# Optimization experiments

Hardware: AMD Instinct MI355X
Metric: run time of the kernel (lower is better)

## Reference

```python
import jax, jax.numpy as jnp
import numpy as np

NUM_HEADS = 16
NUM_KV_HEADS = 4
HEAD_DIM = 128
ROPE_DIMS = 64
EPS = 1.1920929e-07  # torch.finfo(float32).eps, used by F.rms_norm(eps=None)


def rms_norm(x):
    ms = jnp.mean(jnp.square(x), axis=-1, keepdims=True)
    return x * jax.lax.rsqrt(ms + EPS)


def apply_rotary(x, cos, sin):
    # x: [..., s, rope_dims]; cos/sin: [s, rope_dims//2]
    h = x.shape[-1] // 2
    x1, x2 = x[..., :h], x[..., h:]
    return jnp.concatenate([x1 * cos + x2 * sin, -x1 * sin + x2 * cos], axis=-1)


def setup_inputs() -> dict:
    key = jax.random.key(0)
    ks = jax.random.split(key, 5)
    b, s, d = 2, 2048, 2048
    return {
        "x": jax.random.normal(ks[0], (b, s, d), jnp.float32),
        "q_w": jax.random.normal(ks[1], (d, d), jnp.float32) * 0.02,
        "k_w": jax.random.normal(ks[2], (NUM_KV_HEADS * HEAD_DIM, d), jnp.float32) * 0.02,
        "v_w": jax.random.normal(ks[3], (NUM_KV_HEADS * HEAD_DIM, d), jnp.float32) * 0.02,
        "out_w": jax.random.normal(ks[4], (d, d), jnp.float32) * 0.02,
        "q_gain": jnp.full((NUM_HEADS,), 12.0, jnp.float32),
    }


def reference(x, q_w, k_w, v_w, out_w, q_gain):
    b, s, d = x.shape
    g = NUM_HEADS // NUM_KV_HEADS

    q = (x @ q_w.T).reshape(b, s, NUM_HEADS, HEAD_DIM).transpose(0, 2, 1, 3)
    k = (x @ k_w.T).reshape(b, s, NUM_KV_HEADS, HEAD_DIM).transpose(0, 2, 1, 3)
    v = (x @ v_w.T).reshape(b, s, NUM_KV_HEADS, HEAD_DIM).transpose(0, 2, 1, 3)

    q = rms_norm(q)
    k = rms_norm(k)

    # partial rotary embedding
    t = jnp.arange(s, dtype=jnp.float32)
    inv_freq = 1.0 / (10000.0 ** (jnp.arange(0, ROPE_DIMS, 2, dtype=jnp.float32) / ROPE_DIMS))
    f = jnp.outer(t, inv_freq)                      # [s, rope_dims//2]
    cos, sin = jnp.cos(f), jnp.sin(f)

    q = jnp.concatenate([apply_rotary(q[..., :ROPE_DIMS], cos, sin), q[..., ROPE_DIMS:]], axis=-1)
    q = q * q_gain[None, :, None, None]
    k = jnp.concatenate([apply_rotary(k[..., :ROPE_DIMS], cos, sin), k[..., ROPE_DIMS:]], axis=-1)

    # GQA-native causal attention (no repeated K/V materialization)
    qg = q.reshape(b, NUM_KV_HEADS, g, s, HEAD_DIM)
    scale = 1.0 / jnp.sqrt(jnp.float32(HEAD_DIM))
    scores = jnp.einsum("bkgqd,bkld->bkgql", qg, k) * scale
    causal = jnp.tril(jnp.ones((s, s), bool))
    scores = jnp.where(causal, scores, jnp.finfo(scores.dtype).min)
    p = jax.nn.softmax(scores, axis=-1)
    y = jnp.einsum("bkgql,bkld->bkgqd", p, v)       # [b, kvh, g, s, hd]
    y = y.reshape(b, NUM_HEADS, s, HEAD_DIM).transpose(0, 2, 1, 3).reshape(b, s, d)
    return y @ out_w.T
```

## Files before the change

kernel.cpp:

```cpp
#include <hip/hip_runtime.h>
#include <cmath>


#define S_LEN 2048
#define DMODEL 2048
#define NH 16
#define NKV 4
#define HD 128

#define NEG_SENT -1.0e30f
#define QK_SCALE 0.08838834764831845f

typedef _Float16 f16x8 __attribute__((ext_vector_type(8)));
typedef float f32x4 __attribute__((ext_vector_type(4)));

static __device__ __forceinline__ short f2h(float f) {
  _Float16 h = (_Float16)f;
  return *(short*)&h;
}
static __device__ __forceinline__ float h2f(short s) {
  _Float16 h = *(_Float16*)&s;
  return (float)h;
}

__global__ __launch_bounds__(256) void f32_to_f16(const float* __restrict__ src,
                                                  short* __restrict__ dst, int n) {
  int i = (blockIdx.x * 256 + threadIdx.x) * 4;
  if (i < n) {
    float4 v = *reinterpret_cast<const float4*>(src + i);
    short4 o;
    o.x = f2h(v.x); o.y = f2h(v.y); o.z = f2h(v.z); o.w = f2h(v.w);
    *reinterpret_cast<short4*>(dst + i) = o;
  }
}

template <bool F32OUT>
__global__ __launch_bounds__(256) void gemm_bt(const short* __restrict__ A,
                                               const short* __restrict__ W,
                                               void* __restrict__ Cv,
                                               int M, int N, int K) {
  __shared__ __align__(16) short As[128][72];
  __shared__ __align__(16) short Ws[128][72];
  const int tid = threadIdx.x;
  const int wave = tid >> 6, lane = tid & 63;
  const int quad = lane >> 4, l16 = lane & 15;
  const int bm = blockIdx.x * 128, bn = blockIdx.y * 128;
  const int wm = (wave >> 1) * 64, wn = (wave & 1) * 64;

  f32x4 acc[4][4];
#pragma unroll
  for (int i = 0; i < 4; i++)
#pragma unroll
    for (int j = 0; j < 4; j++) acc[i][j] = f32x4{0.f, 0.f, 0.f, 0.f};

  const int lrow = tid >> 3;
  const int lcol = (tid & 7) * 8;

  for (int k0 = 0; k0 < K; k0 += 64) {
    __syncthreads();
#pragma unroll
    for (int i = 0; i < 4; i++) {
      int r = lrow + i * 32;
      *reinterpret_cast<int4*>(&As[r][lcol]) =
          *reinterpret_cast<const int4*>(A + (size_t)(bm + r) * K + k0 + lcol);
      *reinterpret_cast<int4*>(&Ws[r][lcol]) =
          *reinterpret_cast<const int4*>(W + (size_t)(bn + r) * K + k0 + lcol);
    }
    __syncthreads();
#pragma unroll
    for (int kk = 0; kk < 64; kk += 32) {
      f16x8 af[4], bfr[4];
#pragma unroll
      for (int mi = 0; mi < 4; mi++)
        af[mi] = *reinterpret_cast<const f16x8*>(&As[wm + mi * 16 + l16][kk + quad * 8]);
#pragma unroll
      for (int ni = 0; ni < 4; ni++)
        bfr[ni] = *reinterpret_cast<const f16x8*>(&Ws[wn + ni * 16 + l16][kk + quad * 8]);
#pragma unroll
      for (int mi = 0; mi < 4; mi++)
#pragma unroll
        for (int ni = 0; ni < 4; ni++)
          acc[mi][ni] = __builtin_amdgcn_mfma_f32_16x16x32_f16(af[mi], bfr[ni], acc[mi][ni], 0, 0, 0);
    }
  }
#pragma unroll
  for (int mi = 0; mi < 4; mi++)
#pragma unroll
    for (int ni = 0; ni < 4; ni++) {
      int gr = bm + wm + mi * 16 + quad * 4;
      int gc = bn + wn + ni * 16 + l16;
#pragma unroll
      for (int r = 0; r < 4; r++) {
        if (F32OUT)
          ((float*)Cv)[(size_t)(gr + r) * N + gc] = acc[mi][ni][r];
        else
          ((short*)Cv)[(size_t)(gr + r) * N + gc] = f2h(acc[mi][ni][r]);
      }
    }
}

__global__ __launch_bounds__(256) void postproc(const short* __restrict__ src,
                                                short* __restrict__ dst,
                                                const float* __restrict__ gain,
                                                int n_heads, int mode) {
  int gw = blockIdx.x * 4 + (threadIdx.x >> 6);
  int lane = threadIdx.x & 63;
  int head = gw % n_heads;
  int token = gw / n_heads;
  int s = token & (S_LEN - 1);
  int b = token >> 11;
  const short* sp = src + (size_t)token * (n_heads * HD) + head * HD;
  float v0 = h2f(sp[lane]);
  float v1 = h2f(sp[lane + 64]);
  float ss = v0 * v0 + v1 * v1;
#pragma unroll
  for (int off = 1; off < 64; off <<= 1) ss += __shfl_xor(ss, off, 64);
  float sc = rsqrtf(ss * (1.0f / 128.0f) + 1.1920929e-07f);
  v0 *= sc;
  v1 *= sc;
  int i = lane & 31;
  float inv = powf(10000.0f, -((float)(2 * i) * (1.0f / 64.0f)));
  float f = (float)s * inv;
  float cs, sn;
  sincosf(f, &sn, &cs);
  float partner = __shfl_xor(v0, 32, 64);
  v0 = (lane < 32) ? (v0 * cs + partner * sn) : (v0 * cs - partner * sn);
  if (mode == 2) {
    float g = gain[head] * QK_SCALE;
    v0 *= g;
    v1 *= g;
  }
  short* dp = dst + ((size_t)(b * n_heads + head) * S_LEN + s) * HD;
  dp[lane] = f2h(v0);
  dp[lane + 64] = f2h(v1);
}

__global__ __launch_bounds__(256) void v_transpose(const short* __restrict__ src,
                                                   short* __restrict__ dst) {
  __shared__ __align__(16) short t[64][72];
  const int tid = threadIdx.x;
  const int s0 = blockIdx.x * 64;
  const int d0 = blockIdx.y * 64;
#pragma unroll
  for (int i = 0; i < 2; i++) {
    int r = (tid >> 3) + i * 32;
    int c = (tid & 7) * 8;
    *reinterpret_cast<int4*>(&t[r][c]) =
        *reinterpret_cast<const int4*>(src + (size_t)(s0 + r) * 512 + d0 + c);
  }
  __syncthreads();
  const int b = s0 >> 11;
  const int sbase = s0 & (S_LEN - 1);
#pragma unroll
  for (int i = 0; i < 2; i++) {
    int dr = (tid >> 3) + i * 32;
    int sc8 = (tid & 7) * 8;
    int d = d0 + dr;
    int kv = d >> 7, dw = d & 127;
    short4 lo, hi;
    lo.x = t[sc8 + 0][dr]; lo.y = t[sc8 + 1][dr];
    lo.z = t[sc8 + 2][dr]; lo.w = t[sc8 + 3][dr];
    hi.x = t[sc8 + 4][dr]; hi.y = t[sc8 + 5][dr];
    hi.z = t[sc8 + 6][dr]; hi.w = t[sc8 + 7][dr];
    short* dp = dst + (((size_t)(b * NKV + kv) * HD + dw) * S_LEN) + sbase + sc8;
    *reinterpret_cast<short4*>(dp) = lo;
    *reinterpret_cast<short4*>(dp + 4) = hi;
  }
}

__global__ __launch_bounds__(256, 2) void attn_fwd(const short* __restrict__ qb,
                                                   const short* __restrict__ kb,
                                                   const short* __restrict__ vT,
                                                   short* __restrict__ out) {
  __shared__ __align__(16) short k_lds[64][136];
  __shared__ __align__(16) short vt_lds[144][72];
  __shared__ __align__(16) short p_lds[4][16][136];

  const int tid = threadIdx.x, wave = tid >> 6, lane = tid & 63;
  const int quad = lane >> 4, l16 = lane & 15;
  const int bh = blockIdx.y;
  const int b = bh >> 4, h = bh & 15;
  const int kvh = h >> 2;
  const int pj = blockIdx.x;

  const short* kptr = kb + ((size_t)(b * NKV + kvh) * S_LEN) * HD;
  const short* vtp  = vT + ((size_t)(b * NKV + kvh) * HD) * S_LEN;

  const int kr = (tid >> 4), kc = (tid & 15) * 8;
  const int vr = (tid >> 3), vc = (tid & 7) * 8;

  {
    int r = 128 + (tid >> 4);
    int c = (tid & 15) * 4;
    short val = (r == 128) ? (short)0x3C00 : (short)0;
    short4 v4 = {val, val, val, val};
    *reinterpret_cast<short4*>(&vt_lds[r][c]) = v4;
  }

  for (int pass = 0; pass < 2; pass++) {
    const int qsub = pass ? (31 - pj) : pj;
    const int q0 = qsub * 64 + wave * 16;
    const short* qptr = qb + ((size_t)(b * NH + h) * S_LEN + q0) * HD;

    f16x8 qf[4];
#pragma unroll
    for (int st = 0; st < 4; st++)
      qf[st] = *reinterpret_cast<const f16x8*>(
          qptr + (size_t)l16 * HD + st * 32 + quad * 8);

    f32x4 o[9];
#pragma unroll
    for (int i = 0; i < 9; i++) o[i] = f32x4{0.f, 0.f, 0.f, 0.f};
    float m_i[4] = {NEG_SENT, NEG_SENT, NEG_SENT, NEG_SENT};

    const int ktiles = qsub + 1;
    for (int kt = 0; kt < ktiles; kt++) {
      const int kbase = kt * 64;
      __syncthreads();
#pragma unroll
      for (int i = 0; i < 4; i++)
        *reinterpret_cast<int4*>(&k_lds[kr + i * 16][kc]) =
            *reinterpret_cast<const int4*>(kptr + (size_t)(kbase + kr + i * 16) * HD + kc);
#pragma unroll
      for (int i = 0; i < 4; i++)
        *reinterpret_cast<int4*>(&vt_lds[vr + i * 32][vc]) =
            *reinterpret_cast<const int4*>(vtp + (size_t)(vr + i * 32) * S_LEN + kbase + vc);
      __syncthreads();

      f32x4 sc[4];
#pragma unroll
      for (int ct = 0; ct < 4; ct++) sc[ct] = f32x4{0.f, 0.f, 0.f, 0.f};
#pragma unroll
      for (int ct = 0; ct < 4; ct++) {
#pragma unroll
        for (int st = 0; st < 4; st++) {
          f16x8 kf = *reinterpret_cast<const f16x8*>(&k_lds[ct * 16 + l16][st * 32 + quad * 8]);
          sc[ct] = __builtin_amdgcn_mfma_f32_16x16x32_f16(qf[st], kf, sc[ct], 0, 0, 0);
        }
      }

      if (kbase + 63 > q0) {
#pragma unroll
        for (int ct = 0; ct < 4; ct++)
#pragma unroll
          for (int r = 0; r < 4; r++) {
            int qrow = q0 + quad * 4 + r;
            int col = kbase + ct * 16 + l16;
            sc[ct][r] = (col <= qrow) ? sc[ct][r] : NEG_SENT;
          }
      }

      float cand[4];
#pragma unroll
      for (int r = 0; r < 4; r++)
        cand[r] = fmaxf(fmaxf(sc[0][r], sc[1][r]), fmaxf(sc[2][r], sc[3][r]));
#pragma unroll
      for (int off = 1; off < 16; off <<= 1)
#pragma unroll
        for (int r = 0; r < 4; r++)
          cand[r] = fmaxf(cand[r], __shfl_xor(cand[r], off, 64));

      bool ch = (cand[0] > m_i[0]) | (cand[1] > m_i[1]) |
                (cand[2] > m_i[2]) | (cand[3] > m_i[3]);
      if (__any(ch)) {
        float alpha[4];
#pragma unroll
        for (int r = 0; r < 4; r++) {
          float mn = fmaxf(m_i[r], cand[r]);
          alpha[r] = __expf(m_i[r] - mn);
          m_i[r] = mn;
        }
#pragma unroll
        for (int nt = 0; nt < 9; nt++)
#pragma unroll
          for (int r = 0; r < 4; r++) o[nt][r] *= alpha[r];
      }

#pragma unroll
      for (int ct = 0; ct < 4; ct++)
#pragma unroll
        for (int r = 0; r < 4; r++) {
          float p = __expf(sc[ct][r] - m_i[r]);
          p_lds[wave][quad * 4 + r][ct * 16 + l16] = f2h(p);
        }

      f16x8 pf0 = *reinterpret_cast<const f16x8*>(&p_lds[wave][l16][quad * 8]);
      f16x8 pf1 = *reinterpret_cast<const f16x8*>(&p_lds[wave][l16][32 + quad * 8]);
#pragma unroll
      for (int nt = 0; nt < 9; nt++) {
        f16x8 vf0 = *reinterpret_cast<const f16x8*>(&vt_lds[nt * 16 + l16][quad * 8]);
        f16x8 vf1 = *reinterpret_cast<const f16x8*>(&vt_lds[nt * 16 + l16][32 + quad * 8]);
        o[nt] = __builtin_amdgcn_mfma_f32_16x16x32_f16(pf0, vf0, o[nt], 0, 0, 0);
        o[nt] = __builtin_amdgcn_mfma_f32_16x16x32_f16(pf1, vf1, o[nt], 0, 0, 0);
      }
    }

    float inv_l[4];
#pragma unroll
    for (int r = 0; r < 4; r++) {
      float l = __shfl(o[8][r], lane & 48, 64);
      inv_l[r] = 1.0f / fmaxf(l, 1e-20f);
    }
#pragma unroll
    for (int nt = 0; nt < 8; nt++)
#pragma unroll
      for (int r = 0; r < 4; r++) {
        int srow = q0 + quad * 4 + r;
        int dcol = nt * 16 + l16;
        out[((size_t)(b * S_LEN + srow)) * DMODEL + h * HD + dcol] =
            f2h(o[nt][r] * inv_l[r]);
      }
  }
}

extern "C" void kernel_launch(void* const* d_in, const int* in_sizes, int n_in,
                              void* d_out, int out_size, void* d_ws, size_t ws_size,
                              hipStream_t stream) {
  const float* x      = (const float*)d_in[0];
  const float* q_w    = (const float*)d_in[1];
  const float* k_w    = (const float*)d_in[2];
  const float* v_w    = (const float*)d_in[3];
  const float* out_w  = (const float*)d_in[4];
  const float* q_gain = (const float*)d_in[5];
  float* out = (float*)d_out;

  const int BS = 2 * S_LEN;
  short* xb   = (short*)d_ws;
  short* wqb  = xb   + (size_t)8 * 1024 * 1024;
  short* wkb  = wqb  + (size_t)4 * 1024 * 1024;
  short* wvb  = wkb  + (size_t)1 * 1024 * 1024;
  short* wob  = wvb  + (size_t)1 * 1024 * 1024;
  short* qraw = wob  + (size_t)4 * 1024 * 1024;
  short* kraw = qraw + (size_t)8 * 1024 * 1024;
  short* vraw = kraw + (size_t)2 * 1024 * 1024;
  short* qbuf = vraw + (size_t)2 * 1024 * 1024;
  short* kbuf = qbuf + (size_t)8 * 1024 * 1024;
  short* vT   = kbuf + (size_t)2 * 1024 * 1024;
  short* attn = qraw;

  dim3 blk(256);
  f32_to_f16<<<8192, blk, 0, stream>>>(x, xb, BS * DMODEL);
  f32_to_f16<<<4096, blk, 0, stream>>>(q_w, wqb, DMODEL * DMODEL);
  f32_to_f16<<<1024, blk, 0, stream>>>(k_w, wkb, 512 * DMODEL);
  f32_to_f16<<<1024, blk, 0, stream>>>(v_w, wvb, 512 * DMODEL);
  f32_to_f16<<<4096, blk, 0, stream>>>(out_w, wob, DMODEL * DMODEL);

  gemm_bt<false><<<dim3(32, 16), blk, 0, stream>>>(xb, wqb, qraw, 4096, 2048, 2048);
  gemm_bt<false><<<dim3(32, 4), blk, 0, stream>>>(xb, wkb, kraw, 4096, 512, 2048);
  gemm_bt<false><<<dim3(32, 4), blk, 0, stream>>>(xb, wvb, vraw, 4096, 512, 2048);

  postproc<<<dim3((BS * NH) / 4), blk, 0, stream>>>(qraw, qbuf, q_gain, NH, 2);
  postproc<<<dim3((BS * NKV) / 4), blk, 0, stream>>>(kraw, kbuf, q_gain, NKV, 1);
  v_transpose<<<dim3(BS / 64, 8), blk, 0, stream>>>(vraw, vT);

  attn_fwd<<<dim3(16, 2 * NH), blk, 0, stream>>>(qbuf, kbuf, vT, attn);

  gemm_bt<true><<<dim3(32, 16), blk, 0, stream>>>(attn, wob, out, 4096, 2048, 2048);
}
```

Measured before the change: 410.5 us.

## Stage GEMM tiles with direct global-to-LDS loads and merge K/V projections

The GEMM tile loads now use global_load_lds to write 16-byte chunks straight into shared memory, bypassing registers, and the LDS row padding is dropped to fit that layout. The K and V projection GEMMs are combined into one launch using a z-dimension selector. The aim is to cut register traffic and load instructions and to save one kernel launch. The unpadded LDS rows may add bank conflicts on the MFMA fragment reads.

```diff
diff --git a/kernel.cpp b/kernel.cpp
--- a/kernel.cpp
+++ b/kernel.cpp
@@ -21,6 +21,12 @@
 static __device__ __forceinline__ float h2f(short s) {
   _Float16 h = *(_Float16*)&s;
   return (float)h;
+}
+
+static __device__ __forceinline__ void stage16(const short* g, short* ldsbase) {
+  __builtin_amdgcn_global_load_lds(
+      (const __attribute__((address_space(1))) void*)g,
+      (__attribute__((address_space(3))) void*)ldsbase, 16, 0, 0);
 }
 
 __global__ __launch_bounds__(256) void f32_to_f16(const float* __restrict__ src,
@@ -35,16 +41,15 @@
 }
 
 template <bool F32OUT>
-__global__ __launch_bounds__(256) void gemm_bt(const short* __restrict__ A,
-                                               const short* __restrict__ W,
-                                               void* __restrict__ Cv,
-                                               int M, int N, int K) {
-  __shared__ __align__(16) short As[128][72];
-  __shared__ __align__(16) short Ws[128][72];
+static __device__ __forceinline__ void gemm_core(const short* __restrict__ A,
+                                                 const short* __restrict__ W,
+                                                 void* __restrict__ Cv,
+                                                 int N, int K, int bm, int bn) {
+  __shared__ __align__(16) short As[128][64];
+  __shared__ __align__(16) short Ws[128][64];
   const int tid = threadIdx.x;
   const int wave = tid >> 6, lane = tid & 63;
   const int quad = lane >> 4, l16 = lane & 15;
-  const int bm = blockIdx.x * 128, bn = blockIdx.y * 128;
   const int wm = (wave >> 1) * 64, wn = (wave & 1) * 64;
 
   f32x4 acc[4][4];
@@ -53,18 +58,17 @@
 #pragma unroll
     for (int j = 0; j < 4; j++) acc[i][j] = f32x4{0.f, 0.f, 0.f, 0.f};
 
-  const int lrow = tid >> 3;
-  const int lcol = (tid & 7) * 8;
+  const int srow = wave * 8 + (lane >> 3);
+  const int scol = (lane & 7) * 8;
 
   for (int k0 = 0; k0 < K; k0 += 64) {
     __syncthreads();
 #pragma unroll
     for (int i = 0; i < 4; i++) {
-      int r = lrow + i * 32;
-      *reinterpret_cast<int4*>(&As[r][lcol]) =
-          *reinterpret_cast<const int4*>(A + (size_t)(bm + r) * K + k0 + lcol);
-      *reinterpret_cast<int4*>(&Ws[r][lcol]) =
-          *reinterpret_cast<const int4*>(W + (size_t)(bn + r) * K + k0 + lcol);
+      stage16(A + (size_t)(bm + srow + i * 32) * K + k0 + scol,
+              &As[wave * 8 + i * 32][0]);
+      stage16(W + (size_t)(bn + srow + i * 32) * K + k0 + scol,
+              &Ws[wave * 8 + i * 32][0]);
     }
     __syncthreads();
 #pragma unroll
@@ -97,6 +101,25 @@
           ((short*)Cv)[(size_t)(gr + r) * N + gc] = f2h(acc[mi][ni][r]);
       }
     }
+}
+
+template <bool F32OUT>
+__global__ __launch_bounds__(256) void gemm_bt(const short* __restrict__ A,
+                                               const short* __restrict__ W,
+                                               void* __restrict__ Cv,
+                                               int N, int K) {
+  gemm_core<F32OUT>(A, W, Cv, N, K, blockIdx.x * 128, blockIdx.y * 128);
+}
+
+__global__ __launch_bounds__(256) void gemm_kv(const short* __restrict__ A,
+                                               const short* __restrict__ W0,
+                                               const short* __restrict__ W1,
+                                               short* __restrict__ C0,
+                                               short* __restrict__ C1,
+                                               int N, int K) {
+  const short* W = blockIdx.z ? W1 : W0;
+  short* C = blockIdx.z ? C1 : C0;
+  gemm_core<false>(A, W, (void*)C, N, K, blockIdx.x * 128, blockIdx.y * 128);
 }
 
 __global__ __launch_bounds__(256) void postproc(const short* __restrict__ src,
@@ -345,9 +368,8 @@
   f32_to_f16<<<1024, blk, 0, stream>>>(v_w, wvb, 512 * DMODEL);
   f32_to_f16<<<4096, blk, 0, stream>>>(out_w, wob, DMODEL * DMODEL);
 
-  gemm_bt<false><<<dim3(32, 16), blk, 0, stream>>>(xb, wqb, qraw, 4096, 2048, 2048);
-  gemm_bt<false><<<dim3(32, 4), blk, 0, stream>>>(xb, wkb, kraw, 4096, 512, 2048);
-  gemm_bt<false><<<dim3(32, 4), blk, 0, stream>>>(xb, wvb, vraw, 4096, 512, 2048);
+  gemm_bt<false><<<dim3(32, 16), blk, 0, stream>>>(xb, wqb, qraw, 2048, 2048);
+  gemm_kv<<<dim3(32, 4, 2), blk, 0, stream>>>(xb, wkb, wvb, kraw, vraw, 512, 2048);
 
   postproc<<<dim3((BS * NH) / 4), blk, 0, stream>>>(qraw, qbuf, q_gain, NH, 2);
   postproc<<<dim3((BS * NKV) / 4), blk, 0, stream>>>(kraw, kbuf, q_gain, NKV, 1);
@@ -355,5 +377,5 @@
 
   attn_fwd<<<dim3(16, 2 * NH), blk, 0, stream>>>(qbuf, kbuf, vT, attn);
 
-  gemm_bt<true><<<dim3(32, 16), blk, 0, stream>>>(attn, wob, out, 4096, 2048, 2048);
-}
+  gemm_bt<true><<<dim3(32, 16), blk, 0, stream>>>(attn, wob, out, 2048, 2048);
+}
```

Result: faster. 387.1 us (-5.7%).
